# Performance work log

Hardware: AMD Instinct MI355X
Metric: run time of the kernel (lower is better)

The kernel has to match this reference:

```python
import jax, jax.numpy as jnp
import numpy as np

D_MODEL = 256
N_HEADS = 4
SPARSITY_RATIO = 0.5
B, N, E = 4, 2048, 65536


def setup_inputs() -> dict:
    key = jax.random.key(0)
    ks = jax.random.split(key, 16)
    d, h = D_MODEL, D_MODEL // 2
    s = 1.0 / np.sqrt(d)
    inp = {
        "x": jax.random.normal(ks[0], (B, N, d), dtype=jnp.float32),
        "edge_index": jax.random.randint(ks[1], (2, E), 0, N, dtype=jnp.int64),
        "Wq": jax.random.uniform(ks[2], (d, d), minval=-s, maxval=s),
        "bq": jnp.zeros((d,), jnp.float32),
        "Wk": jax.random.uniform(ks[3], (d, d), minval=-s, maxval=s),
        "bk": jnp.zeros((d,), jnp.float32),
        "Wv": jax.random.uniform(ks[4], (d, d), minval=-s, maxval=s),
        "bv": jnp.zeros((d,), jnp.float32),
        "Wo": jax.random.uniform(ks[5], (d, d), minval=-s, maxval=s),
        "bo": jnp.zeros((d,), jnp.float32),
        "Wg1": jax.random.uniform(ks[6], (d, h), minval=-s, maxval=s),  # gnn conv1 (in,out)
        "bg1": jnp.zeros((h,), jnp.float32),
        "Wg2": jax.random.uniform(ks[7], (h, 1), minval=-s, maxval=s),  # gnn conv2
        "bg2": jnp.zeros((1,), jnp.float32),
    }
    return inp


def reference(x, edge_index, Wq, bq, Wk, bk, Wv, bv, Wo, bo, Wg1, bg1, Wg2, bg2):
    b, n, d = x.shape
    hd = d // N_HEADS
    row, col = edge_index[0], edge_index[1]

    # Lightweight GNN topo scores, vmapped over batch (replaces python loop)
    def gnn(xb):
        aggr = jax.ops.segment_sum(xb[col], row, num_segments=n)  # [N, d]
        hdn = jax.nn.relu(aggr @ Wg1 + bg1)
        return (hdn @ Wg2 + bg2)[:, 0]  # [N]

    topo_scores = jax.vmap(gnn)(x)  # [B, N]

    Q = (x @ Wq + bq).reshape(b, n, N_HEADS, hd)
    K = (x @ Wk + bk).reshape(b, n, N_HEADS, hd)
    V = (x @ Wv + bv).reshape(b, n, N_HEADS, hd)

    content_scores = jnp.einsum('bnhd,bmhd->bhnm', Q, K) / np.sqrt(hd)
    content_attn = jax.nn.softmax(content_scores, axis=-1)  # [B,H,N,N]

    # Edge mask (identical across batch, assignment semantics => set)
    edge_mask = jnp.zeros((n, n), jnp.float32).at[row, col].set(1.0)

    # top-k columns per batch (same columns for every query row i)
    k = max(1, int(n * (1 - SPARSITY_RATIO)))
    _, topk_idx = jax.lax.top_k(topo_scores, k)  # [B, k]
    col_mask = jnp.zeros((b, n), jnp.float32).at[jnp.arange(b)[:, None], topk_idx].set(1.0)

    sparse_mask = jnp.maximum(edge_mask[None, :, :], col_mask[:, None, :])  # [B,N,N]
    mask4 = jnp.broadcast_to(sparse_mask[:, None, :, :], (b, N_HEADS, n, n))

    sparse_attn = content_attn * mask4
    sparse_attn = sparse_attn / (jnp.sum(sparse_attn, axis=-1, keepdims=True) + 1e-8)

    out = jnp.einsum('bhnm,bmhd->bnhd', sparse_attn, V).reshape(b, n, d)
    out = out @ Wo + bo
    return out, mask4
```

## Files before the change

kernel.cpp:

```cpp
#include <hip/hip_runtime.h>
#include <hip/hip_bf16.h>
#include <stdint.h>

#define NTOK 2048
#define NB 4
#define DM 256
#define HD 64
#define NE 65536
#define SCAP 128
#define NKSL 4
#define ROWS_A 2112
#define ROWS_B 6272

typedef __bf16 bf16x8 __attribute__((ext_vector_type(8)));
typedef float f32x4 __attribute__((ext_vector_type(4)));

#define MFMA16 __builtin_amdgcn_mfma_f32_16x16x32_bf16

__device__ __forceinline__ unsigned short f2bf(float f) {
    union { float f; uint32_t u; } v; v.f = f;
    return (unsigned short)((v.u + 0x7fffu + ((v.u >> 16) & 1u)) >> 16);
}

__global__ __launch_bounds__(256) void k_prep(const float* __restrict__ x,
                       unsigned short* __restrict__ xb,
                       const float* __restrict__ W0, const float* __restrict__ W1,
                       const float* __restrict__ W2, const float* __restrict__ W3,
                       unsigned short* __restrict__ WT, float4* __restrict__ wsz,
                       const float* __restrict__ Wg1, float* __restrict__ y) {
    __shared__ float xs[16][256];
    int bid = blockIdx.x, t = threadIdx.x;
    if (bid < 132) {
        wsz[bid * 256 + t] = float4{0.f, 0.f, 0.f, 0.f};
    } else if (bid < 1156) {
        int b2 = bid - 132;
        int sel = b2 >> 8;
        const float* W = sel == 0 ? W0 : sel == 1 ? W1 : sel == 2 ? W2 : W3;
        int e = (b2 & 255) * 256 + t;
        int n = e >> 8, k = e & 255;
        WT[sel * 65536 + e] = f2bf(W[k * 256 + n]);
    } else {
        int m0 = (bid - 1156) * 16;
        #pragma unroll
        for (int j = 0; j < 16; ++j) {
            float v = x[(size_t)(m0 + j) * DM + t];
            xs[j][t] = v;
            xb[(size_t)(m0 + j) * DM + t] = f2bf(v);
        }
        __syncthreads();
        int c = t & 127, g = t >> 7;
        float acc[8] = {0.f, 0.f, 0.f, 0.f, 0.f, 0.f, 0.f, 0.f};
        const float* xr = &xs[g * 8][0];
        #pragma unroll 4
        for (int r = 0; r < DM; ++r) {
            float w = Wg1[r * 128 + c];
            #pragma unroll
            for (int j = 0; j < 8; ++j) acc[j] += xr[j * 256 + r] * w;
        }
        #pragma unroll
        for (int j = 0; j < 8; ++j) y[(size_t)(m0 + g * 8 + j) * 128 + c] = acc[j];
    }
}

__global__ void k_edges(const int* __restrict__ ei, uint32_t* __restrict__ cursor,
                        uint32_t* __restrict__ scol, uint32_t* __restrict__ ebits) {
    int e = blockIdx.x * 256 + threadIdx.x;
    int r = ei[e];
    int c = ei[NE + e];
    uint32_t slot = atomicAdd(&cursor[r], 1u);
    if (slot < SCAP) scol[r * SCAP + slot] = (uint32_t)c;
    atomicOr(&ebits[r * 64 + (c >> 5)], 1u << (c & 31));
}

__global__ __launch_bounds__(256) void k_gnn_qkv(
    const float* __restrict__ y, const uint32_t* __restrict__ cursor,
    const uint32_t* __restrict__ scol,
    const float* __restrict__ bg1, const float* __restrict__ Wg2,
    const float* __restrict__ bg2, float* __restrict__ topo,
    const unsigned short* __restrict__ xbf, const unsigned short* __restrict__ WT,
    const float* __restrict__ bq, const float* __restrict__ bk, const float* __restrict__ bv,
    unsigned short* __restrict__ qo, unsigned short* __restrict__ kt,
    unsigned short* __restrict__ vt3) {
    int bid = blockIdx.x, t = threadIdx.x;
    if (bid < 2048) {
        int i = bid;
        int d = t & 127, bp = t >> 7;
        uint32_t cnt = cursor[i]; if (cnt > SCAP) cnt = SCAP;
        const uint32_t* sc = scol + i * SCAP;
        const float* yA = y + (size_t)(bp * NTOK) * 128 + d;
        const float* yB = y + (size_t)((bp + 2) * NTOK) * 128 + d;
        double A0 = 0, A1 = 0, A2 = 0, A3 = 0;
        double B0 = 0, B1 = 0, B2 = 0, B3 = 0;
        uint32_t e = 0;
        for (; e + 3 < cnt; e += 4) {
            int c0 = sc[e] << 7, c1 = sc[e + 1] << 7;
            int c2 = sc[e + 2] << 7, c3 = sc[e + 3] << 7;
            A0 += (double)yA[c0]; A1 += (double)yA[c1];
            A2 += (double)yA[c2]; A3 += (double)yA[c3];
            B0 += (double)yB[c0]; B1 += (double)yB[c1];
            B2 += (double)yB[c2]; B3 += (double)yB[c3];
        }
        for (; e < cnt; ++e) {
            int c0 = sc[e] << 7;
            A0 += (double)yA[c0];
            B0 += (double)yB[c0];
        }
        double hA = (A0 + A1) + (A2 + A3) + (double)bg1[d];
        double hB = (B0 + B1) + (B2 + B3) + (double)bg1[d];
        double w2 = (double)Wg2[d];
        double vA = (hA > 0 ? hA : 0.0) * w2;
        double vB = (hB > 0 ? hB : 0.0) * w2;
        #pragma unroll
        for (int s = 32; s >= 1; s >>= 1) {
            vA += __shfl_xor(vA, s);
            vB += __shfl_xor(vB, s);
        }
        __shared__ double red[4][2];
        int wid = t >> 6;
        if ((t & 63) == 0) { red[wid][0] = vA; red[wid][1] = vB; }
        __syncthreads();
        if (t == 0) {
            double bb = (double)bg2[0];
            topo[0 * NTOK + i] = (float)(red[0][0] + red[1][0] + bb);
            topo[2 * NTOK + i] = (float)(red[0][1] + red[1][1] + bb);
            topo[1 * NTOK + i] = (float)(red[2][0] + red[3][0] + bb);
            topo[3 * NTOK + i] = (float)(red[2][1] + red[3][1] + bb);
        }
    } else {
        int b2 = bid - 2048;
        int z = b2 >> 9, r2 = b2 & 511;
        const unsigned short* W = WT + z * 65536;
        const float* bias = z == 0 ? bq : z == 1 ? bk : bv;

        int lane = t & 63, w = t >> 6;
        int l15 = lane & 15, grp = lane >> 4;
        int mbase = (r2 & 127) * 64 + w * 16;
        int nbase = (r2 >> 7) * 64;
        f32x4 acc0 = {0,0,0,0}, acc1 = {0,0,0,0}, acc2 = {0,0,0,0}, acc3 = {0,0,0,0};
        const unsigned short* ap = xbf + (size_t)(mbase + l15) * DM + grp * 8;
        const unsigned short* bp2 = W + (size_t)(nbase + l15) * DM + grp * 8;
        #pragma unroll
        for (int k0 = 0; k0 < DM; k0 += 32) {
            bf16x8 af = *(const bf16x8*)(ap + k0);
            acc0 = MFMA16(af, *(const bf16x8*)(bp2 + k0), acc0, 0, 0, 0);
            acc1 = MFMA16(af, *(const bf16x8*)(bp2 + 16 * DM + k0), acc1, 0, 0, 0);
            acc2 = MFMA16(af, *(const bf16x8*)(bp2 + 32 * DM + k0), acc2, 0, 0, 0);
            acc3 = MFMA16(af, *(const bf16x8*)(bp2 + 48 * DM + k0), acc3, 0, 0, 0);
        }
        f32x4 accs[4] = {acc0, acc1, acc2, acc3};
        #pragma unroll
        for (int ct = 0; ct < 4; ++ct) {
            #pragma unroll
            for (int r = 0; r < 4; ++r) {
                int m = mbase + grp * 4 + r;
                int n = nbase + ct * 16 + l15;
                float v = accs[ct][r] + bias[n];
                if (z == 0) {
                    qo[(size_t)m * DM + n] = f2bf(v);
                } else {
                    int b = m >> 11, tok = m & 2047, h = n >> 6, d = n & 63;
                    int bh = (b << 2) + h;
                    if (z == 1) {
                        kt[(size_t)bh * 131072 + (tok >> 4) * 1024 + (tok & 15) * 64 + d] = f2bf(v);
                    } else {
                        vt3[(size_t)bh * 131072 + (tok >> 5) * 2048 + d * 32 + (tok & 31)] = f2bf(v);
                    }
                }
            }
        }
    }
}

__global__ __launch_bounds__(256) void k_topk(const float* __restrict__ topo,
                                              uint32_t* __restrict__ colbits) {
    int b = blockIdx.y, t = threadIdx.x;
    int i = blockIdx.x * 256 + t;
    __shared__ float4 sc4[NTOK / 4];
    const float4* tp = (const float4*)(topo + b * NTOK);
    for (int j = t; j < NTOK / 4; j += 256) sc4[j] = tp[j];
    __syncthreads();
    float si = ((const float*)sc4)[i];
    int rank = 0;
    #pragma unroll 2
    for (int jj = 0; jj < NTOK / 4; ++jj) {
        float4 v = sc4[jj];
        int j0 = jj * 4;
        rank += (v.x > si) || (v.x == si && (j0    ) < i);
        rank += (v.y > si) || (v.y == si && (j0 + 1) < i);
        rank += (v.z > si) || (v.z == si && (j0 + 2) < i);
        rank += (v.w > si) || (v.w == si && (j0 + 3) < i);
    }
    unsigned long long m = __ballot(rank < 1024);
    int lane = t & 63;
    if (lane == 0)       colbits[b * 64 + (i >> 5)] = (uint32_t)m;
    else if (lane == 32) colbits[b * 64 + (i >> 5)] = (uint32_t)(m >> 32);
}

__device__ __forceinline__ void mask_row(int rowidx, const uint32_t* __restrict__ eb,
                                         const uint32_t* __restrict__ cb,
                                         float* __restrict__ mout) {
    int t = threadIdx.x;
    int b = rowidx >> 13;
    int i = rowidx & 2047;
    int j0 = t << 3;
    uint32_t mw = eb[i * 64 + (j0 >> 5)] | cb[b * 64 + (j0 >> 5)];
    int sh = j0 & 31;
    float4 v0, v1;
    v0.x = ((mw >> sh) & 1u) ? 1.f : 0.f;
    v0.y = ((mw >> (sh + 1)) & 1u) ? 1.f : 0.f;
    v0.z = ((mw >> (sh + 2)) & 1u) ? 1.f : 0.f;
    v0.w = ((mw >> (sh + 3)) & 1u) ? 1.f : 0.f;
    v1.x = ((mw >> (sh + 4)) & 1u) ? 1.f : 0.f;
    v1.y = ((mw >> (sh + 5)) & 1u) ? 1.f : 0.f;
    v1.z = ((mw >> (sh + 6)) & 1u) ? 1.f : 0.f;
    v1.w = ((mw >> (sh + 7)) & 1u) ? 1.f : 0.f;
    float* p = mout + (size_t)rowidx * NTOK + j0;
    *(float4*)p = v0;
    *(float4*)(p + 4) = v1;
}

__global__ __launch_bounds__(256) void k_attn_mask(const unsigned short* __restrict__ Q,
                                                   const unsigned short* __restrict__ KT,
                                                   const unsigned short* __restrict__ VT3,
                                                   const uint32_t* __restrict__ ebits,
                                                   const uint32_t* __restrict__ colbits,
                                                   float* __restrict__ po,
                                                   float* __restrict__ pl,
                                                   float* __restrict__ mout) {
    int bid = blockIdx.x;
    if (bid >= 2048) {
        mask_row(bid - 2048 + ROWS_B, ebits, colbits, mout);
        return;
    }
    __shared__ unsigned short ksh[2][2048];
    __shared__ unsigned short vsh[2][2048];
    int t = threadIdx.x;
    int lane = t & 63, w = t >> 6;
    int l15 = lane & 15, grp = lane >> 4;
    int ks = bid >> 9;
    int bh = (bid >> 5) & 15, b = bh >> 2, h = bh & 3;
    int q = (bid & 31) * 64 + w * 16 + l15;

    const unsigned short* qp = Q + (size_t)(b * NTOK + q) * DM + h * HD + grp * 8;
    bf16x8 qf0 = *(const bf16x8*)(qp);
    bf16x8 qf1 = *(const bf16x8*)(qp + 32);
    const unsigned short* Kt = KT + (size_t)bh * 131072;
    const unsigned short* Vt = VT3 + (size_t)bh * 131072;
    const uint32_t* eb = ebits + q * 64;
    const uint32_t* cbp = colbits + b * 64;

    int kb0 = ks * (NTOK / NKSL);
    int kso = (t * 16) ^ (((t >> 3) & 7) << 4);
    int vso = (t * 16) ^ (((t >> 2) & 7) << 4);
    int swz = (l15 & 7) << 4;

    {
        uint4 kv = *(const uint4*)(Kt + (size_t)(kb0 >> 4) * 1024 + t * 8);
        *(uint4*)((char*)&ksh[0][0] + kso) = kv;
        uint4 vv = *(const uint4*)(Vt + (size_t)(kb0 >> 5) * 2048 + t * 8);
        *(uint4*)((char*)&vsh[0][0] + vso) = vv;
    }
    __syncthreads();

    f32x4 o0 = {0,0,0,0}, o1 = {0,0,0,0}, o2 = {0,0,0,0}, o3 = {0,0,0,0};
    float psum = 0.f;

    for (int it = 0; it < NTOK / NKSL / 32; ++it) {
        int buf = it & 1;
        if (it + 1 < NTOK / NKSL / 32) {
            int kb = kb0 + (it + 1) * 32;
            uint4 kv = *(const uint4*)(Kt + (size_t)(kb >> 4) * 1024 + t * 8);
            *(uint4*)((char*)&ksh[buf ^ 1][0] + kso) = kv;
            uint4 vv = *(const uint4*)(Vt + (size_t)(kb >> 5) * 2048 + t * 8);
            *(uint4*)((char*)&vsh[buf ^ 1][0] + vso) = vv;
        }
        int kb = kb0 + it * 32;
        const char* kp = (const char*)&ksh[buf][0];
        const char* vp = (const char*)&vsh[buf][0];

        f32x4 st0 = {0,0,0,0}, st1 = {0,0,0,0};
        st0 = MFMA16(*(const bf16x8*)(kp + ((l15 * 128 + grp * 16) ^ swz)),        qf0, st0, 0, 0, 0);
        st0 = MFMA16(*(const bf16x8*)(kp + ((l15 * 128 + 64 + grp * 16) ^ swz)),   qf1, st0, 0, 0, 0);
        st1 = MFMA16(*(const bf16x8*)(kp + (((16 + l15) * 128 + grp * 16) ^ swz)), qf0, st1, 0, 0, 0);
        st1 = MFMA16(*(const bf16x8*)(kp + (((16 + l15) * 128 + 64 + grp * 16) ^ swz)), qf1, st1, 0, 0, 0);

        uint32_t mw = eb[kb >> 5] | cbp[kb >> 5];
        float p[8];
        #pragma unroll
        for (int r = 0; r < 4; ++r) {
            int p0 = grp * 4 + r;
            p[r]     = ((mw >> p0) & 1u)        ? __expf(st0[r] * 0.125f - 8.0f) : 0.f;
            p[4 + r] = ((mw >> (16 + p0)) & 1u) ? __expf(st1[r] * 0.125f - 8.0f) : 0.f;
        }
        #pragma unroll
        for (int j = 0; j < 8; ++j) psum += p[j];

        uint32_t pk00, pk01, pk10, pk11;
        asm("v_cvt_pk_bf16_f32 %0, %1, %2" : "=v"(pk00) : "v"(p[0]), "v"(p[1]));
        asm("v_cvt_pk_bf16_f32 %0, %1, %2" : "=v"(pk01) : "v"(p[2]), "v"(p[3]));
        asm("v_cvt_pk_bf16_f32 %0, %1, %2" : "=v"(pk10) : "v"(p[4]), "v"(p[5]));
        asm("v_cvt_pk_bf16_f32 %0, %1, %2" : "=v"(pk11) : "v"(p[6]), "v"(p[7]));
        union { uint32_t u[4]; bf16x8 v; } pf;
        #pragma unroll
        for (int wi = 0; wi < 4; ++wi) {
            int src = (((grp * 2 + (wi >> 1)) & 3) << 4) | l15;
            uint32_t lo = (uint32_t)__shfl((int)((wi & 1) ? pk01 : pk00), src);
            uint32_t hi = (uint32_t)__shfl((int)((wi & 1) ? pk11 : pk10), src);
            pf.u[wi] = (lane >= 32) ? hi : lo;
        }

        o0 = MFMA16(*(const bf16x8*)(vp + ((l15 * 64 + grp * 16) ^ swz)),          pf.v, o0, 0, 0, 0);
        o1 = MFMA16(*(const bf16x8*)(vp + (((16 + l15) * 64 + grp * 16) ^ swz)),   pf.v, o1, 0, 0, 0);
        o2 = MFMA16(*(const bf16x8*)(vp + (((32 + l15) * 64 + grp * 16) ^ swz)),   pf.v, o2, 0, 0, 0);
        o3 = MFMA16(*(const bf16x8*)(vp + (((48 + l15) * 64 + grp * 16) ^ swz)),   pf.v, o3, 0, 0, 0);
        __syncthreads();
    }
    psum += __shfl_xor(psum, 16);
    psum += __shfl_xor(psum, 32);

    float* pb = po + (((size_t)(ks * 16 + bh) * NTOK + q) * HD);
    *(f32x4*)(pb + 0 * 16 + grp * 4) = o0;
    *(f32x4*)(pb + 1 * 16 + grp * 4) = o1;
    *(f32x4*)(pb + 2 * 16 + grp * 4) = o2;
    *(f32x4*)(pb + 3 * 16 + grp * 4) = o3;
    if (grp == 0) pl[(size_t)(ks * 16 + bh) * NTOK + q] = psum;
}

__global__ __launch_bounds__(256) void k_fin(const float* __restrict__ po,
                                             const float* __restrict__ pl,
                                             unsigned short* __restrict__ aoutb) {
    const size_t SL = (size_t)16 * NTOK * HD;
    const size_t SLP = (size_t)16 * NTOK;
    int tid = blockIdx.x * 256 + threadIdx.x;
    int dc = tid & 7;
    int q = (tid >> 3) & 2047;
    int bh = tid >> 14;
    size_t rb = ((size_t)bh * NTOK + q) * HD + dc * 8;
    float4 s0 = *(const float4*)(po + rb);
    float4 s1 = *(const float4*)(po + rb + 4);
    #pragma unroll
    for (int ks = 1; ks < NKSL; ++ks) {
        float4 a = *(const float4*)(po + ks * SL + rb);
        float4 c = *(const float4*)(po + ks * SL + rb + 4);
        s0.x += a.x; s0.y += a.y; s0.z += a.z; s0.w += a.w;
        s1.x += c.x; s1.y += c.y; s1.z += c.z; s1.w += c.w;
    }
    float l = 0.f;
    #pragma unroll
    for (int ks = 0; ks < NKSL; ++ks) l += pl[ks * SLP + (size_t)bh * NTOK + q];
    float inv = 1.f / l;
    int b = bh >> 2, h = bh & 3;
    union { ushort4 u4[2]; uint4 v; } out;
    out.u4[0].x = f2bf(s0.x * inv); out.u4[0].y = f2bf(s0.y * inv);
    out.u4[0].z = f2bf(s0.z * inv); out.u4[0].w = f2bf(s0.w * inv);
    out.u4[1].x = f2bf(s1.x * inv); out.u4[1].y = f2bf(s1.y * inv);
    out.u4[1].z = f2bf(s1.z * inv); out.u4[1].w = f2bf(s1.w * inv);
    *(uint4*)(aoutb + ((size_t)(b * NTOK + q) * DM) + h * HD + dc * 8) = out.v;
}

__device__ __forceinline__ void gemm_o_body(int bid, const unsigned short* __restrict__ A,
                                            const unsigned short* __restrict__ WT,
                                            const float* __restrict__ bias,
                                            float* __restrict__ out) {
    int lane = threadIdx.x & 63, w = threadIdx.x >> 6;
    int l15 = lane & 15, grp = lane >> 4;
    int mbase = (bid & 127) * 64 + w * 16;
    int nbase = (bid >> 7) * 64;
    f32x4 acc0 = {0,0,0,0}, acc1 = {0,0,0,0}, acc2 = {0,0,0,0}, acc3 = {0,0,0,0};
    const unsigned short* ap = A + (size_t)(mbase + l15) * DM + grp * 8;
    const unsigned short* bp = WT + (size_t)(nbase + l15) * DM + grp * 8;
    #pragma unroll
    for (int k0 = 0; k0 < DM; k0 += 32) {
        bf16x8 af = *(const bf16x8*)(ap + k0);
        acc0 = MFMA16(af, *(const bf16x8*)(bp + k0), acc0, 0, 0, 0);
        acc1 = MFMA16(af, *(const bf16x8*)(bp + 16 * DM + k0), acc1, 0, 0, 0);
        acc2 = MFMA16(af, *(const bf16x8*)(bp + 32 * DM + k0), acc2, 0, 0, 0);
        acc3 = MFMA16(af, *(const bf16x8*)(bp + 48 * DM + k0), acc3, 0, 0, 0);
    }
    f32x4 accs[4] = {acc0, acc1, acc2, acc3};
    #pragma unroll
    for (int ct = 0; ct < 4; ++ct) {
        #pragma unroll
        for (int r = 0; r < 4; ++r) {
            int m = mbase + grp * 4 + r;
            int n = nbase + ct * 16 + l15;
            out[(size_t)m * DM + n] = accs[ct][r] + bias[n];
        }
    }
}

__global__ __launch_bounds__(256) void k_gemm_mask(const unsigned short* __restrict__ A,
                                                   const unsigned short* __restrict__ WT,
                                                   const float* __restrict__ bias,
                                                   float* __restrict__ out,
                                                   const uint32_t* __restrict__ ebits,
                                                   const uint32_t* __restrict__ colbits,
                                                   float* __restrict__ mout) {
    int bid = blockIdx.x;
    if (bid < 512) {
        gemm_o_body(bid, A, WT, bias, out);
    } else {
        mask_row(bid - 512 + ROWS_A, ebits, colbits, mout);
    }
}

__global__ void k_mask4b(const uint32_t* __restrict__ ebits, const uint32_t* __restrict__ colbits,
                         float* __restrict__ mout) {
    mask_row(blockIdx.x, ebits, colbits, mout);
}

extern "C" void kernel_launch(void* const* d_in, const int* in_sizes, int n_in,
                              void* d_out, int out_size, void* d_ws, size_t ws_size,
                              hipStream_t stream) {
    const float* x   = (const float*)d_in[0];
    const int*   ei  = (const int*)d_in[1];
    const float* Wq  = (const float*)d_in[2];
    const float* bq  = (const float*)d_in[3];
    const float* Wk  = (const float*)d_in[4];
    const float* bk  = (const float*)d_in[5];
    const float* Wv  = (const float*)d_in[6];
    const float* bv  = (const float*)d_in[7];
    const float* Wo  = (const float*)d_in[8];
    const float* bo  = (const float*)d_in[9];
    const float* Wg1 = (const float*)d_in[10];
    const float* bg1 = (const float*)d_in[11];
    const float* Wg2 = (const float*)d_in[12];
    const float* bg2 = (const float*)d_in[13];

    float* out0  = (float*)d_out;
    float* mask4 = out0 + (size_t)NB * NTOK * DM;

    uint8_t* big = (uint8_t*)mask4;
    unsigned short* qbf   = (unsigned short*)(big);
    unsigned short* kt    = (unsigned short*)(big + (4u  << 20));
    unsigned short* vt3   = (unsigned short*)(big + (8u  << 20));
    unsigned short* wt    = (unsigned short*)(big + (12u << 20));
    unsigned short* aoutb = (unsigned short*)(big + (12u << 20) + (512u << 10));
    float*          po    = (float*)         (big + (16u << 20) + (512u << 10));
    float*          pl    = (float*)         (big + (48u << 20) + (512u << 10));
    unsigned short* xbf   = (unsigned short*)(big + (49u << 20));
    uint32_t*       scol  = (uint32_t*)      (big + (53u << 20));
    float*          y     = (float*)         (big + (54u << 20));

    uint8_t* ws = (uint8_t*)d_ws;
    uint32_t* cursor  = (uint32_t*)(ws);
    uint32_t* ebits   = (uint32_t*)(ws + (16u << 10));
    uint32_t* colbits = (uint32_t*)(ws + (528u << 10));
    float*    topo    = (float*)(ws + (532u << 10));

    k_prep<<<1668, 256, 0, stream>>>(x, xbf, Wq, Wk, Wv, Wo, wt, (float4*)ws, Wg1, y);
    k_edges<<<256, 256, 0, stream>>>(ei, cursor, scol, ebits);
    k_gnn_qkv<<<3584, 256, 0, stream>>>(y, cursor, scol, bg1, Wg2, bg2, topo,
                                        xbf, wt, bq, bk, bv, qbf, kt, vt3);
    k_topk<<<dim3(8, 4), 256, 0, stream>>>(topo, colbits);
    k_attn_mask<<<2048 + (32768 - ROWS_B), 256, 0, stream>>>(qbf, kt, vt3, ebits, colbits,
                                                             po, pl, mask4);
    k_fin<<<1024, 256, 0, stream>>>(po, pl, aoutb);
    k_gemm_mask<<<512 + (ROWS_B - ROWS_A), 256, 0, stream>>>(aoutb, wt + 196608, bo, out0,
                                                             ebits, colbits, mask4);
    k_mask4b<<<ROWS_A, 256, 0, stream>>>(ebits, colbits, mask4);
}
```

Baseline: 242.5 us.

## Store split-K attention partials in bf16 and repack scratch to shrink mask tail

The split-K attention partial outputs are now written as bf16 instead of fp32, which halves both the write and the re-read traffic in the finalize step. The scratch buffers living inside the mask output region are repacked more compactly, so more mask rows can be written early, alongside the attention, finalize and output-GEMM kernels. Fewer rows are then left for the final standalone mask kernel. The edge-scatter kernel is merged into the prep kernel, and a small zeroing kernel now runs first. The trade-off is bf16 rounding of the partial sums before the cross-slice reduction, which adds some precision loss.

```diff
diff --git a/kernel.cpp b/kernel.cpp
--- a/kernel.cpp
+++ b/kernel.cpp
@@ -9,8 +9,9 @@
 #define NE 65536
 #define SCAP 128
 #define NKSL 4
-#define ROWS_A 2112
-#define ROWS_B 6272
+#define ROWS_W   576
+#define ROWS_PO  2688
+#define ROWS_QKV 4224
 
 typedef __bf16 bf16x8 __attribute__((ext_vector_type(8)));
 typedef float f32x4 __attribute__((ext_vector_type(4)));
@@ -22,25 +23,28 @@
     return (unsigned short)((v.u + 0x7fffu + ((v.u >> 16) & 1u)) >> 16);
 }
 
-__global__ __launch_bounds__(256) void k_prep(const float* __restrict__ x,
+__global__ void k_zero(float4* __restrict__ p) {
+    p[blockIdx.x * 256 + threadIdx.x] = float4{0.f, 0.f, 0.f, 0.f};
+}
+
+__global__ __launch_bounds__(256) void k_prep_edges(const float* __restrict__ x,
                        unsigned short* __restrict__ xb,
                        const float* __restrict__ W0, const float* __restrict__ W1,
                        const float* __restrict__ W2, const float* __restrict__ W3,
-                       unsigned short* __restrict__ WT, float4* __restrict__ wsz,
-                       const float* __restrict__ Wg1, float* __restrict__ y) {
+                       unsigned short* __restrict__ WT,
+                       const float* __restrict__ Wg1, float* __restrict__ y,
+                       const int* __restrict__ ei, uint32_t* __restrict__ cursor,
+                       uint32_t* __restrict__ scol, uint32_t* __restrict__ ebits) {
     __shared__ float xs[16][256];
     int bid = blockIdx.x, t = threadIdx.x;
-    if (bid < 132) {
-        wsz[bid * 256 + t] = float4{0.f, 0.f, 0.f, 0.f};
-    } else if (bid < 1156) {
-        int b2 = bid - 132;
-        int sel = b2 >> 8;
+    if (bid < 1024) {
+        int sel = bid >> 8;
         const float* W = sel == 0 ? W0 : sel == 1 ? W1 : sel == 2 ? W2 : W3;
-        int e = (b2 & 255) * 256 + t;
+        int e = (bid & 255) * 256 + t;
         int n = e >> 8, k = e & 255;
         WT[sel * 65536 + e] = f2bf(W[k * 256 + n]);
-    } else {
-        int m0 = (bid - 1156) * 16;
+    } else if (bid < 1536) {
+        int m0 = (bid - 1024) * 16;
         #pragma unroll
         for (int j = 0; j < 16; ++j) {
             float v = x[(size_t)(m0 + j) * DM + t];
@@ -59,17 +63,14 @@
         }
         #pragma unroll
         for (int j = 0; j < 8; ++j) y[(size_t)(m0 + g * 8 + j) * 128 + c] = acc[j];
-    }
-}
-
-__global__ void k_edges(const int* __restrict__ ei, uint32_t* __restrict__ cursor,
-                        uint32_t* __restrict__ scol, uint32_t* __restrict__ ebits) {
-    int e = blockIdx.x * 256 + threadIdx.x;
-    int r = ei[e];
-    int c = ei[NE + e];
-    uint32_t slot = atomicAdd(&cursor[r], 1u);
-    if (slot < SCAP) scol[r * SCAP + slot] = (uint32_t)c;
-    atomicOr(&ebits[r * 64 + (c >> 5)], 1u << (c & 31));
+    } else {
+        int e = (bid - 1536) * 256 + t;
+        int r = ei[e];
+        int c = ei[NE + e];
+        uint32_t slot = atomicAdd(&cursor[r], 1u);
+        if (slot < SCAP) scol[r * SCAP + slot] = (uint32_t)c;
+        atomicOr(&ebits[r * 64 + (c >> 5)], 1u << (c & 31));
+    }
 }
 
 __global__ __launch_bounds__(256) void k_gnn_qkv(
@@ -224,12 +225,12 @@
                                                    const unsigned short* __restrict__ VT3,
                                                    const uint32_t* __restrict__ ebits,
                                                    const uint32_t* __restrict__ colbits,
-                                                   float* __restrict__ po,
+                                                   unsigned short* __restrict__ po16,
                                                    float* __restrict__ pl,
                                                    float* __restrict__ mout) {
     int bid = blockIdx.x;
     if (bid >= 2048) {
-        mask_row(bid - 2048 + ROWS_B, ebits, colbits, mout);
+        mask_row(bid - 2048 + ROWS_QKV, ebits, colbits, mout);
         return;
     }
     __shared__ unsigned short ksh[2][2048];
@@ -318,32 +319,44 @@
     psum += __shfl_xor(psum, 16);
     psum += __shfl_xor(psum, 32);
 
-    float* pb = po + (((size_t)(ks * 16 + bh) * NTOK + q) * HD);
-    *(f32x4*)(pb + 0 * 16 + grp * 4) = o0;
-    *(f32x4*)(pb + 1 * 16 + grp * 4) = o1;
-    *(f32x4*)(pb + 2 * 16 + grp * 4) = o2;
-    *(f32x4*)(pb + 3 * 16 + grp * 4) = o3;
+    unsigned short* pb = po16 + (((size_t)(ks * 16 + bh) * NTOK + q) * HD);
+    uint32_t c0, c1;
+    asm("v_cvt_pk_bf16_f32 %0, %1, %2" : "=v"(c0) : "v"(o0[0]), "v"(o0[1]));
+    asm("v_cvt_pk_bf16_f32 %0, %1, %2" : "=v"(c1) : "v"(o0[2]), "v"(o0[3]));
+    *(uint2*)(pb + grp * 4) = make_uint2(c0, c1);
+    asm("v_cvt_pk_bf16_f32 %0, %1, %2" : "=v"(c0) : "v"(o1[0]), "v"(o1[1]));
+    asm("v_cvt_pk_bf16_f32 %0, %1, %2" : "=v"(c1) : "v"(o1[2]), "v"(o1[3]));
+    *(uint2*)(pb + 16 + grp * 4) = make_uint2(c0, c1);
+    asm("v_cvt_pk_bf16_f32 %0, %1, %2" : "=v"(c0) : "v"(o2[0]), "v"(o2[1]));
+    asm("v_cvt_pk_bf16_f32 %0, %1, %2" : "=v"(c1) : "v"(o2[2]), "v"(o2[3]));
+    *(uint2*)(pb + 32 + grp * 4) = make_uint2(c0, c1);
+    asm("v_cvt_pk_bf16_f32 %0, %1, %2" : "=v"(c0) : "v"(o3[0]), "v"(o3[1]));
+    asm("v_cvt_pk_bf16_f32 %0, %1, %2" : "=v"(c1) : "v"(o3[2]), "v"(o3[3]));
+    *(uint2*)(pb + 48 + grp * 4) = make_uint2(c0, c1);
     if (grp == 0) pl[(size_t)(ks * 16 + bh) * NTOK + q] = psum;
 }
 
-__global__ __launch_bounds__(256) void k_fin(const float* __restrict__ po,
-                                             const float* __restrict__ pl,
-                                             unsigned short* __restrict__ aoutb) {
+__device__ __forceinline__ void fin_body(int tid, const unsigned short* __restrict__ po16,
+                                         const float* __restrict__ pl,
+                                         unsigned short* __restrict__ aoutb) {
     const size_t SL = (size_t)16 * NTOK * HD;
     const size_t SLP = (size_t)16 * NTOK;
-    int tid = blockIdx.x * 256 + threadIdx.x;
     int dc = tid & 7;
     int q = (tid >> 3) & 2047;
     int bh = tid >> 14;
     size_t rb = ((size_t)bh * NTOK + q) * HD + dc * 8;
-    float4 s0 = *(const float4*)(po + rb);
-    float4 s1 = *(const float4*)(po + rb + 4);
+    float s[8] = {0.f, 0.f, 0.f, 0.f, 0.f, 0.f, 0.f, 0.f};
     #pragma unroll
-    for (int ks = 1; ks < NKSL; ++ks) {
-        float4 a = *(const float4*)(po + ks * SL + rb);
-        float4 c = *(const float4*)(po + ks * SL + rb + 4);
-        s0.x += a.x; s0.y += a.y; s0.z += a.z; s0.w += a.w;
-        s1.x += c.x; s1.y += c.y; s1.z += c.z; s1.w += c.w;
+    for (int ks = 0; ks < NKSL; ++ks) {
+        uint4 v = *(const uint4*)(po16 + ks * SL + rb);
+        s[0] += __uint_as_float(v.x << 16);
+        s[1] += __uint_as_float(v.x & 0xffff0000u);
+        s[2] += __uint_as_float(v.y << 16);
+        s[3] += __uint_as_float(v.y & 0xffff0000u);
+        s[4] += __uint_as_float(v.z << 16);
+        s[5] += __uint_as_float(v.z & 0xffff0000u);
+        s[6] += __uint_as_float(v.w << 16);
+        s[7] += __uint_as_float(v.w & 0xffff0000u);
     }
     float l = 0.f;
     #pragma unroll
@@ -351,11 +364,25 @@
     float inv = 1.f / l;
     int b = bh >> 2, h = bh & 3;
     union { ushort4 u4[2]; uint4 v; } out;
-    out.u4[0].x = f2bf(s0.x * inv); out.u4[0].y = f2bf(s0.y * inv);
-    out.u4[0].z = f2bf(s0.z * inv); out.u4[0].w = f2bf(s0.w * inv);
-    out.u4[1].x = f2bf(s1.x * inv); out.u4[1].y = f2bf(s1.y * inv);
-    out.u4[1].z = f2bf(s1.z * inv); out.u4[1].w = f2bf(s1.w * inv);
+    out.u4[0].x = f2bf(s[0] * inv); out.u4[0].y = f2bf(s[1] * inv);
+    out.u4[0].z = f2bf(s[2] * inv); out.u4[0].w = f2bf(s[3] * inv);
+    out.u4[1].x = f2bf(s[4] * inv); out.u4[1].y = f2bf(s[5] * inv);
+    out.u4[1].z = f2bf(s[6] * inv); out.u4[1].w = f2bf(s[7] * inv);
     *(uint4*)(aoutb + ((size_t)(b * NTOK + q) * DM) + h * HD + dc * 8) = out.v;
+}
+
+__global__ __launch_bounds__(256) void k_fin_mask(const unsigned short* __restrict__ po16,
+                                                  const float* __restrict__ pl,
+                                                  unsigned short* __restrict__ aoutb,
+                                                  const uint32_t* __restrict__ ebits,
+                                                  const uint32_t* __restrict__ colbits,
+                                                  float* __restrict__ mout) {
+    int bid = blockIdx.x;
+    if (bid < 1024) {
+        fin_body(bid * 256 + threadIdx.x, po16, pl, aoutb);
+    } else {
+        mask_row(bid - 1024 + ROWS_PO, ebits, colbits, mout);
+    }
 }
 
 __device__ __forceinline__ void gemm_o_body(int bid, const unsigned short* __restrict__ A,
@@ -400,7 +427,7 @@
     if (bid < 512) {
         gemm_o_body(bid, A, WT, bias, out);
     } else {
-        mask_row(bid - 512 + ROWS_A, ebits, colbits, mout);
+        mask_row(bid - 512 + ROWS_W, ebits, colbits, mout);
     }
 }
 
@@ -431,16 +458,16 @@
     float* mask4 = out0 + (size_t)NB * NTOK * DM;
 
     uint8_t* big = (uint8_t*)mask4;
-    unsigned short* qbf   = (unsigned short*)(big);
-    unsigned short* kt    = (unsigned short*)(big + (4u  << 20));
-    unsigned short* vt3   = (unsigned short*)(big + (8u  << 20));
-    unsigned short* wt    = (unsigned short*)(big + (12u << 20));
-    unsigned short* aoutb = (unsigned short*)(big + (12u << 20) + (512u << 10));
-    float*          po    = (float*)         (big + (16u << 20) + (512u << 10));
-    float*          pl    = (float*)         (big + (48u << 20) + (512u << 10));
-    unsigned short* xbf   = (unsigned short*)(big + (49u << 20));
-    uint32_t*       scol  = (uint32_t*)      (big + (53u << 20));
-    float*          y     = (float*)         (big + (54u << 20));
+    unsigned short* wt    = (unsigned short*)(big);
+    unsigned short* aoutb = (unsigned short*)(big + (512u << 10));
+    unsigned short* po16  = (unsigned short*)(big + (4u  << 20) + (512u << 10));
+    float*          pl    = (float*)         (big + (20u << 20) + (512u << 10));
+    unsigned short* qbf   = (unsigned short*)(big + (21u << 20));
+    unsigned short* kt    = (unsigned short*)(big + (25u << 20));
+    unsigned short* vt3   = (unsigned short*)(big + (29u << 20));
+    unsigned short* xbf   = (unsigned short*)(big + (33u << 20));
+    uint32_t*       scol  = (uint32_t*)      (big + (37u << 20));
+    float*          y     = (float*)         (big + (38u << 20));
 
     uint8_t* ws = (uint8_t*)d_ws;
     uint32_t* cursor  = (uint32_t*)(ws);
@@ -448,15 +475,17 @@
     uint32_t* colbits = (uint32_t*)(ws + (528u << 10));
     float*    topo    = (float*)(ws + (532u << 10));
 
-    k_prep<<<1668, 256, 0, stream>>>(x, xbf, Wq, Wk, Wv, Wo, wt, (float4*)ws, Wg1, y);
-    k_edges<<<256, 256, 0, stream>>>(ei, cursor, scol, ebits);
+    k_zero<<<132, 256, 0, stream>>>((float4*)ws);
+    k_prep_edges<<<1792, 256, 0, stream>>>(x, xbf, Wq, Wk, Wv, Wo, wt, Wg1, y,
+                                           ei, cursor, scol, ebits);
     k_gnn_qkv<<<3584, 256, 0, stream>>>(y, cursor, scol, bg1, Wg2, bg2, topo,
                                         xbf, wt, bq, bk, bv, qbf, kt, vt3);
     k_topk<<<dim3(8, 4), 256, 0, stream>>>(topo, colbits);
-    k_attn_mask<<<2048 + (32768 - ROWS_B), 256, 0, stream>>>(qbf, kt, vt3, ebits, colbits,
-                                                             po, pl, mask4);
-    k_fin<<<1024, 256, 0, stream>>>(po, pl, aoutb);
-    k_gemm_mask<<<512 + (ROWS_B - ROWS_A), 256, 0, stream>>>(aoutb, wt + 196608, bo, out0,
-                                                             ebits, colbits, mask4);
-    k_mask4b<<<ROWS_A, 256, 0, stream>>>(ebits, colbits, mask4);
-}
+    k_attn_mask<<<2048 + (32768 - ROWS_QKV), 256, 0, stream>>>(qbf, kt, vt3, ebits, colbits,
+                                                               po16, pl, mask4);
+    k_fin_mask<<<1024 + (ROWS_QKV - ROWS_PO), 256, 0, stream>>>(po16, pl, aoutb,
+                                                                ebits, colbits, mask4);
+    k_gemm_mask<<<512 + (ROWS_PO - ROWS_W), 256, 0, stream>>>(aoutb, wt + 196608, bo, out0,
+                                                              ebits, colbits, mask4);
+    k_mask4b<<<ROWS_W, 256, 0, stream>>>(ebits, colbits, mask4);
+}
```

After: 246.3 us. No clear change (+1.6%).
